# Optimization experiments

Measured on AMD Instinct MI355X. Metric: run time of the kernel, lower is better.

## Reference

```python
import jax, jax.numpy as jnp
import numpy as np
import math

STD = math.exp(0.0025)  # exp(0.5 * 0.005) from log_sigma = 0.005
C = 0.5 * math.log(2 * math.pi)
B, X, H, Z, L, W = 8192, 512, 256, 64, 16, 32

def _predict(h, Wd, bd, Wo, bo):
    return jax.nn.sigmoid(jax.nn.relu(h @ Wd.T + bd) @ Wo.T + bo)

def _gru(xin, h, Wih, Whh, bih, bhh):
    gi = xin @ Wih.T + bih
    gh = h @ Whh.T + bhh
    ir, iz, inn = jnp.split(gi, 3, axis=1)
    hr, hz, hn = jnp.split(gh, 3, axis=1)
    r = jax.nn.sigmoid(ir + hr)
    zt = jax.nn.sigmoid(iz + hz)
    n = jnp.tanh(inn + r * hn)
    return (1.0 - zt) * n + zt * h

def setup_inputs():
    key = jax.random.key(0)
    ks = iter(jax.random.split(key, 40))
    def nrm(shape, s=0.05):
        return jax.random.normal(next(ks), shape, dtype=jnp.float32) * s
    return {
        "x": jax.random.uniform(next(ks), (B, X), dtype=jnp.float32),
        "workers": jax.random.uniform(next(ks), (W, B, L), dtype=jnp.float32),
        "Wf1": nrm((H, X)), "bf1": jnp.zeros((H,)),
        "Wf2": nrm((1, H)), "bf2": jnp.zeros((1,)),
        "eWih": nrm((L, 3 * H, X + 1)), "eWhh": nrm((L, 3 * H, H)),
        "ebih": jnp.zeros((L, 3 * H)), "ebhh": jnp.zeros((L, 3 * H)),
        "eWd": nrm((L, H, H)), "ebd": jnp.zeros((L, H)),
        "eWo": nrm((L, 1, H)), "ebo": jnp.zeros((L, 1)),
        "Wmu": nrm((Z, H)), "bmu": jnp.zeros((Z,)),
        "Wlv": nrm((Z, H)), "blv": jnp.zeros((Z,)),
        "dWih": nrm((L, 3 * H, Z + 1)), "dWhh": nrm((L, 3 * H, H)),
        "dbih": jnp.zeros((L, 3 * H)), "dbhh": jnp.zeros((L, 3 * H)),
        "dWd": nrm((L, H, H)), "dbd": jnp.zeros((L, H)),
        "dWo": nrm((L, W, H)), "dbo": jnp.zeros((L, W)),
        "Wr": nrm((X, H)), "br": jnp.zeros((X,)),
        "enc_eps": jax.random.normal(next(ks), (L, B, H), dtype=jnp.float32),
        "samp_eps": jax.random.normal(next(ks), (B, Z), dtype=jnp.float32),
        "dec_eps": jax.random.uniform(next(ks), (L, B, H), dtype=jnp.float32),
    }

def _forward(x, workers, Wf1, bf1, Wf2, bf2, eWih, eWhh, ebih, ebhh, eWd, ebd, eWo, ebo,
             Wmu, bmu, Wlv, blv, dWih, dWhh, dbih, dbhh, dWd, dbd, dWo, dbo, Wr, br,
             enc_eps, samp_eps, dec_eps):
    nB = x.shape[0]
    h_dim = eWhh.shape[2]
    # Encoder: t[:,0] = firstcell(x)
    t0 = _predict(x, Wf1, bf1, Wf2, bf2)[:, 0]
    z0 = jnp.zeros((nB, h_dim), dtype=x.dtype)

    def enc_step(carry, xs):
        z, ti = carry
        Wih, Whh, bih, bhh, Wd, bd, Wo, bo, eps = xs
        tmp = (ti >= 0.5).astype(x.dtype)
        mu = _gru(jnp.concatenate([x, tmp[:, None]], axis=1), z, Wih, Whh, bih, bhh)
        znew = mu + STD * eps
        tn = _predict(znew, Wd, bd, Wo, bo)[:, 0]
        return (znew, tn), ti

    (z_fin, _), tcols = jax.lax.scan(
        enc_step, (z0, t0), (eWih, eWhh, ebih, ebhh, eWd, ebd, eWo, ebo, enc_eps))
    t = tcols.T  # [B, L]
    mu_z = z_fin @ Wmu.T + bmu
    log_var = jax.nn.softplus(z_fin @ Wlv.T + blv)
    latent = mu_z + jnp.exp(0.5 * log_var) * samp_eps
    tmp_t = (t > 0.5).astype(x.dtype)

    def dec_step(zt, xs):
        Wih, Whh, bih, bhh, Wd, bd, Wo, bo, tcol, eps = xs
        mu = _gru(jnp.concatenate([latent, tcol[:, None]], axis=1), zt, Wih, Whh, bih, bhh)
        znew = mu + STD * eps  # decoder uses uniform eps (torch.rand)
        return znew, _predict(znew, Wd, bd, Wo, bo)

    zT, preds = jax.lax.scan(
        dec_step, jnp.zeros((nB, h_dim), dtype=x.dtype),
        (dWih, dWhh, dbih, dbhh, dWd, dbd, dWo, dbo, tmp_t.T, dec_eps))
    worker_preds = jnp.transpose(preds, (2, 1, 0))  # [L,B,W] -> [W,B,L]
    recon = jax.nn.sigmoid(zT @ Wr.T + br)
    log_p_x = jnp.sum(x * jnp.log(recon), axis=1)
    logp = jnp.clip(jnp.log(worker_preds), -100.0)
    log1mp = jnp.clip(jnp.log1p(-worker_preds), -100.0)
    bce = -(workers * logp + (1.0 - workers) * log1mp)
    log_p_y = -jnp.sum(jnp.sum(bce, axis=0), axis=1)
    workers_bar = jnp.mean(workers, axis=0)
    log_kl = jnp.sum(t * (jnp.log(t + 1e-6) - jnp.log(workers_bar + 1e-6)), axis=1)
    log_p_z = jnp.sum(-C - latent ** 2 / 2, axis=-1)
    log_q = jnp.sum(-C - log_var / 2 - (latent - mu_z) ** 2 / (2 * jnp.exp(log_var)), axis=-1)
    loss = jnp.mean(log_q - log_p_z - log_p_y - log_p_x + log_kl)
    return t, loss

def reference(x, workers, Wf1, bf1, Wf2, bf2, eWih, eWhh, ebih, ebhh, eWd, ebd, eWo, ebo,
              Wmu, bmu, Wlv, blv, dWih, dWhh, dbih, dbhh, dWd, dbd, dWo, dbo, Wr, br,
              enc_eps, samp_eps, dec_eps):
    return _forward(x, workers, Wf1, bf1, Wf2, bf2, eWih, eWhh, ebih, ebhh, eWd, ebd,
                    eWo, ebo, Wmu, bmu, Wlv, blv, dWih, dWhh, dbih, dbhh, dWd, dbd,
                    dWo, dbo, Wr, br, enc_eps, samp_eps, dec_eps)
```

## Files before the change

### kernel.cpp

```cpp
#include <hip/hip_runtime.h>
#include <hip/hip_bf16.h>
#include <math.h>

#define B_ 8192
#define X_ 512
#define H_ 256
#define Z_ 64
#define L_ 16
#define W_ 32
#define G3_ 768

#define STDF 1.0025031276057952f
#define CC 0.9189385332046727f

typedef _Float16 f16x8 __attribute__((ext_vector_type(8)));
typedef float f32x4 __attribute__((ext_vector_type(4)));

__device__ __forceinline__ float sigm(float x) { return 1.0f / (1.0f + expf(-x)); }
__device__ __forceinline__ float logsig(float u) {
    return (u > 0.0f) ? -log1pf(expf(-u)) : (u - log1pf(expf(u)));
}

#define GLOAD16(gsrc, ldst) \
    __builtin_amdgcn_global_load_lds((const __attribute__((address_space(1))) unsigned int*)(gsrc), \
                                     (__attribute__((address_space(3))) unsigned int*)(ldst), 16, 0, 0)

#define WAITV(N) asm volatile("s_waitcnt vmcnt(" #N ")" ::: "memory")
#define SBAR()  do { __builtin_amdgcn_sched_barrier(0); __builtin_amdgcn_s_barrier(); } while (0)

template<int BN>
__global__ __launch_bounds__(256) void mfma_gemm(
    const _Float16* __restrict__ A,
    const _Float16* __restrict__ Wt,
    const float* __restrict__ bias,
    float* __restrict__ C, int ldc,
    int K, int act)
{
    constexpr int BM = 128;
    constexpr int WN = BN / 2;
    constexpr int NFR = WN / 16;
    __shared__ char smem[2][(BM + BN) * 128];

    const int tid  = threadIdx.x;
    const int wave = tid >> 6;
    const int lane = tid & 63;
    const int wr   = wave >> 1;
    const int wc   = wave & 1;
    const int bm   = blockIdx.y * BM;
    const int bn   = blockIdx.x * BN;
    const int l15  = lane & 15;
    const int l4   = lane >> 4;

    f32x4 acc[4][NFR];
    #pragma unroll
    for (int a = 0; a < 4; ++a)
        #pragma unroll
        for (int b = 0; b < NFR; ++b) {
            f32x4 zz = {0.f, 0.f, 0.f, 0.f};
            acc[a][b] = zz;
        }

    auto stage = [&](int s, int pb) {
        char* As = smem[pb];
        char* Ws = smem[pb] + BM * 128;
        int k0 = s * 64;
        #pragma unroll
        for (int it = 0; it < 4; ++it) {
            int q   = it * 4 + wave;
            int o   = q * 1024 + lane * 16;
            int row = o >> 7;
            int c   = ((o >> 4) & 7) ^ (row & 7);
            GLOAD16(A + (long)(bm + row) * K + k0 + c * 8, As + q * 1024);
        }
        #pragma unroll
        for (int it = 0; it < BN / 32; ++it) {
            int q   = it * 4 + wave;
            int o   = q * 1024 + lane * 16;
            int row = o >> 7;
            int c   = ((o >> 4) & 7) ^ (row & 7);
            GLOAD16(Wt + (long)(bn + row) * K + k0 + c * 8, Ws + q * 1024);
        }
    };

    const int NT = K >> 6;
    stage(0, 0);
    for (int s = 0; s < NT; ++s) {
        int pb = s & 1;
        if (s + 1 < NT) {
            stage(s + 1, pb ^ 1);
            if constexpr (BN == 128) WAITV(8); else WAITV(6);
        } else WAITV(0);
        SBAR();
        char* As = smem[pb];
        char* Ws = smem[pb] + BM * 128;
        #pragma unroll
        for (int ks = 0; ks < 2; ++ks) {
            f16x8 af[4], bf[NFR];
            #pragma unroll
            for (int mi = 0; mi < 4; ++mi) {
                int row = wr * 64 + mi * 16 + l15;
                int c   = (ks * 4 + l4) ^ (row & 7);
                af[mi] = *(const f16x8*)(As + row * 128 + c * 16);
            }
            #pragma unroll
            for (int ni = 0; ni < NFR; ++ni) {
                int row = wc * WN + ni * 16 + l15;
                int c   = (ks * 4 + l4) ^ (row & 7);
                bf[ni] = *(const f16x8*)(Ws + row * 128 + c * 16);
            }
            #pragma unroll
            for (int mi = 0; mi < 4; ++mi)
                #pragma unroll
                for (int ni = 0; ni < NFR; ++ni)
                    acc[mi][ni] = __builtin_amdgcn_mfma_f32_16x16x32_f16(
                        af[mi], bf[ni], acc[mi][ni], 0, 0, 0);
        }
        SBAR();
    }

    #pragma unroll
    for (int mi = 0; mi < 4; ++mi)
        #pragma unroll
        for (int r = 0; r < 4; ++r) {
            int grow = bm + wr * 64 + mi * 16 + l4 * 4 + r;
            #pragma unroll
            for (int ni = 0; ni < NFR; ++ni) {
                int gcol = bn + wc * WN + ni * 16 + l15;
                float v = acc[mi][ni][r] + bias[gcol];
                if (act) v = fmaxf(v, 0.0f);
                C[(long)grow * ldc + gcol] = v;
            }
        }
}

template<int MODE, int KX, int FIRST>
__global__ __launch_bounds__(256) void gru_fused(
    const _Float16* __restrict__ A2,
    const _Float16* __restrict__ Wih,
    const float* __restrict__ bih,
    const _Float16* __restrict__ Whh,
    const float* __restrict__ bhh,
    const float* __restrict__ ec,
    const float* __restrict__ tcol,
    const float* __restrict__ eps,
    const _Float16* __restrict__ zh_in,
    float* __restrict__ z,
    _Float16* __restrict__ zh_out)
{
    constexpr int N1 = KX / 64;
    constexpr int NT = N1 + (FIRST ? 0 : 4);
    __shared__ char smem[2][(64 + 192) * 128];

    const int tid  = threadIdx.x;
    const int wave = tid >> 6;
    const int lane = tid & 63;
    const int wr   = wave >> 1;
    const int wc   = wave & 1;
    const int id   = blockIdx.x;
    const int xcd  = id & 7;
    const int wk   = id >> 3;
    const int bm   = (xcd * 16 + (wk >> 2)) * 64;
    const int h0   = (wk & 3) * 64;
    const int l15  = lane & 15;
    const int l4   = lane >> 4;

    f32x4 acc[2][6];
    f32x4 accN[2][2];
    #pragma unroll
    for (int a = 0; a < 2; ++a) {
        #pragma unroll
        for (int b = 0; b < 6; ++b) { f32x4 zz = {0.f,0.f,0.f,0.f}; acc[a][b] = zz; }
        #pragma unroll
        for (int b = 0; b < 2; ++b) { f32x4 zz = {0.f,0.f,0.f,0.f}; accN[a][b] = zz; }
    }

    auto stage = [&](int s, int pb) {
        char* As = smem[pb];
        char* Ws = smem[pb] + 64 * 128;
        const _Float16* srcA;
        const _Float16* srcW;
        int KA, k0;
        if (s < N1) { srcA = A2;    srcW = Wih; KA = KX;  k0 = s * 64; }
        else        { srcA = zh_in; srcW = Whh; KA = 256; k0 = (s - N1) * 64; }
        #pragma unroll
        for (int it = 0; it < 2; ++it) {
            int q   = it * 4 + wave;
            int o   = q * 1024 + lane * 16;
            int row = o >> 7;
            int c   = ((o >> 4) & 7) ^ (row & 7);
            GLOAD16(srcA + (long)(bm + row) * KA + k0 + c * 8, As + q * 1024);
        }
        #pragma unroll
        for (int it = 0; it < 6; ++it) {
            int q   = it * 4 + wave;
            int o   = q * 1024 + lane * 16;
            int rr  = o >> 7;
            int c   = ((o >> 4) & 7) ^ (rr & 7);
            int srow = (rr >> 6) * 256 + h0 + (rr & 63);
            GLOAD16(srcW + (long)srow * KA + k0 + c * 8, Ws + q * 1024);
        }
    };

    stage(0, 0);
    for (int s = 0; s < NT; ++s) {
        int pb = s & 1;
        if (s + 1 < NT) { stage(s + 1, pb ^ 1); WAITV(8); }
        else WAITV(0);
        SBAR();
        char* As = smem[pb];
        char* Ws = smem[pb] + 64 * 128;
        bool p1 = (s < N1);
        #pragma unroll
        for (int ks = 0; ks < 2; ++ks) {
            f16x8 af[2], bf[6];
            #pragma unroll
            for (int mi = 0; mi < 2; ++mi) {
                int row = wr * 32 + mi * 16 + l15;
                int c   = (ks * 4 + l4) ^ (row & 7);
                af[mi] = *(const f16x8*)(As + row * 128 + c * 16);
            }
            #pragma unroll
            for (int ni = 0; ni < 6; ++ni) {
                int rr = (ni >> 1) * 64 + wc * 32 + (ni & 1) * 16 + l15;
                int c  = (ks * 4 + l4) ^ (rr & 7);
                bf[ni] = *(const f16x8*)(Ws + rr * 128 + c * 16);
            }
            if (p1) {
                #pragma unroll
                for (int mi = 0; mi < 2; ++mi) {
                    #pragma unroll
                    for (int ni = 0; ni < 4; ++ni)
                        acc[mi][ni] = __builtin_amdgcn_mfma_f32_16x16x32_f16(
                            af[mi], bf[ni], acc[mi][ni], 0, 0, 0);
                    #pragma unroll
                    for (int ni = 4; ni < 6; ++ni)
                        accN[mi][ni - 4] = __builtin_amdgcn_mfma_f32_16x16x32_f16(
                            af[mi], bf[ni], accN[mi][ni - 4], 0, 0, 0);
                }
            } else {
                #pragma unroll
                for (int mi = 0; mi < 2; ++mi)
                    #pragma unroll
                    for (int ni = 0; ni < 6; ++ni)
                        acc[mi][ni] = __builtin_amdgcn_mfma_f32_16x16x32_f16(
                            af[mi], bf[ni], acc[mi][ni], 0, 0, 0);
            }
        }
        SBAR();
    }

    #pragma unroll
    for (int mi = 0; mi < 2; ++mi)
        #pragma unroll
        for (int r = 0; r < 4; ++r) {
            int grow = bm + wr * 32 + mi * 16 + l4 * 4 + r;
            float tv = tcol[(long)grow * L_];
            float ext = (MODE == 1) ? (tv >= 0.5f ? 1.0f : 0.0f)
                                    : (tv >  0.5f ? 1.0f : 0.0f);
            #pragma unroll
            for (int hb = 0; hb < 2; ++hb) {
                int h = h0 + wc * 32 + hb * 16 + l15;
                float rpre = acc[mi][hb][r]     + bih[h]       + bhh[h]       + ext * ec[h];
                float zpre = acc[mi][2 + hb][r] + bih[256 + h] + bhh[256 + h] + ext * ec[256 + h];
                float hn   = acc[mi][4 + hb][r] + bhh[512 + h];
                float in_  = accN[mi][hb][r]    + bih[512 + h] + ext * ec[512 + h];
                float rg = sigm(rpre);
                float zt = sigm(zpre);
                float n  = tanhf(in_ + rg * hn);
                long zi = (long)grow * 256 + h;
                float zold = FIRST ? 0.0f : z[zi];
                float v = (1.0f - zt) * n + zt * zold + STDF * eps[zi];
                z[zi] = v;
                zh_out[zi] = (_Float16)v;
            }
        }
}

template<int K>
__global__ __launch_bounds__(256) void predict_head(
    const _Float16* __restrict__ A,
    const _Float16* __restrict__ Wd,
    const float* __restrict__ bd,
    const float* __restrict__ wo,
    const float* __restrict__ bo,
    float* __restrict__ out, int ostride)
{
    constexpr int NT = K / 64;
    __shared__ char smem[2][(32 + 256) * 128];
    __shared__ float part[32][4];

    const int tid  = threadIdx.x;
    const int wave = tid >> 6;
    const int lane = tid & 63;
    const int bm   = blockIdx.x * 32;
    const int l15  = lane & 15;
    const int l4   = lane >> 4;

    f32x4 acc[2][4];
    #pragma unroll
    for (int a = 0; a < 2; ++a)
        #pragma unroll
        for (int b = 0; b < 4; ++b) { f32x4 zz = {0.f,0.f,0.f,0.f}; acc[a][b] = zz; }

    auto stage = [&](int s, int pb) {
        char* As = smem[pb];
        char* Ws = smem[pb] + 32 * 128;
        int k0 = s * 64;
        {
            int o   = wave * 1024 + lane * 16;
            int row = o >> 7;
            int c   = ((o >> 4) & 7) ^ (row & 7);
            GLOAD16(A + (long)(bm + row) * K + k0 + c * 8, As + wave * 1024);
        }
        #pragma unroll
        for (int it = 0; it < 8; ++it) {
            int q   = it * 4 + wave;
            int o   = q * 1024 + lane * 16;
            int row = o >> 7;
            int c   = ((o >> 4) & 7) ^ (row & 7);
            GLOAD16(Wd + (long)row * K + k0 + c * 8, Ws + q * 1024);
        }
    };

    stage(0, 0);
    for (int s = 0; s < NT; ++s) {
        int pb = s & 1;
        if (s + 1 < NT) { stage(s + 1, pb ^ 1); WAITV(9); }
        else WAITV(0);
        SBAR();
        char* As = smem[pb];
        char* Ws = smem[pb] + 32 * 128;
        #pragma unroll
        for (int ks = 0; ks < 2; ++ks) {
            f16x8 af[2], bf[4];
            #pragma unroll
            for (int mi = 0; mi < 2; ++mi) {
                int row = mi * 16 + l15;
                int c   = (ks * 4 + l4) ^ (row & 7);
                af[mi] = *(const f16x8*)(As + row * 128 + c * 16);
            }
            #pragma unroll
            for (int ni = 0; ni < 4; ++ni) {
                int row = wave * 64 + ni * 16 + l15;
                int c   = (ks * 4 + l4) ^ (row & 7);
                bf[ni] = *(const f16x8*)(Ws + row * 128 + c * 16);
            }
            #pragma unroll
            for (int mi = 0; mi < 2; ++mi)
                #pragma unroll
                for (int ni = 0; ni < 4; ++ni)
                    acc[mi][ni] = __builtin_amdgcn_mfma_f32_16x16x32_f16(
                        af[mi], bf[ni], acc[mi][ni], 0, 0, 0);
        }
        SBAR();
    }

    float bdv[4], wov[4];
    #pragma unroll
    for (int ni = 0; ni < 4; ++ni) {
        int col = wave * 64 + ni * 16 + l15;
        bdv[ni] = bd[col];
        wov[ni] = wo[col];
    }
    #pragma unroll
    for (int mi = 0; mi < 2; ++mi)
        #pragma unroll
        for (int r = 0; r < 4; ++r) {
            float s = 0.0f;
            #pragma unroll
            for (int ni = 0; ni < 4; ++ni) {
                float v = fmaxf(acc[mi][ni][r] + bdv[ni], 0.0f);
                s = fmaf(v, wov[ni], s);
            }
            #pragma unroll
            for (int off = 1; off < 16; off <<= 1) s += __shfl_xor(s, off, 16);
            if (l15 == 0) part[mi * 16 + l4 * 4 + r][wave] = s;
        }
    __syncthreads();
    if (tid < 32) {
        float u = part[tid][0] + part[tid][1] + part[tid][2] + part[tid][3] + bo[0];
        out[(long)(bm + tid) * ostride] = sigm(u);
    }
}

__global__ __launch_bounds__(256) void dec_head_bce(
    const _Float16* __restrict__ A,
    const _Float16* __restrict__ Wd,
    const float* __restrict__ bd,
    const _Float16* __restrict__ Wo,
    const float* __restrict__ bo,
    const float* __restrict__ wt,
    float* __restrict__ bacc)
{
    constexpr int NT = 4;
    __shared__ char smem[2][(32 + 256) * 128];
    __shared__ _Float16 ds[32 * 264];
    __shared__ float part[32][2];

    const int tid  = threadIdx.x;
    const int wave = tid >> 6;
    const int lane = tid & 63;
    const int bm   = blockIdx.x * 32;
    const int l15  = lane & 15;
    const int l4   = lane >> 4;

    f32x4 acc[2][4];
    #pragma unroll
    for (int a = 0; a < 2; ++a)
        #pragma unroll
        for (int b = 0; b < 4; ++b) { f32x4 zz = {0.f,0.f,0.f,0.f}; acc[a][b] = zz; }

    auto stage = [&](int s, int pb) {
        char* As = smem[pb];
        char* Ws = smem[pb] + 32 * 128;
        int k0 = s * 64;
        {
            int o   = wave * 1024 + lane * 16;
            int row = o >> 7;
            int c   = ((o >> 4) & 7) ^ (row & 7);
            GLOAD16(A + (long)(bm + row) * 256 + k0 + c * 8, As + wave * 1024);
        }
        #pragma unroll
        for (int it = 0; it < 8; ++it) {
            int q   = it * 4 + wave;
            int o   = q * 1024 + lane * 16;
            int row = o >> 7;
            int c   = ((o >> 4) & 7) ^ (row & 7);
            GLOAD16(Wd + (long)row * 256 + k0 + c * 8, Ws + q * 1024);
        }
    };

    stage(0, 0);
    for (int s = 0; s < NT; ++s) {
        int pb = s & 1;
        if (s + 1 < NT) { stage(s + 1, pb ^ 1); WAITV(9); }
        else WAITV(0);
        SBAR();
        char* As = smem[pb];
        char* Ws = smem[pb] + 32 * 128;
        #pragma unroll
        for (int ks = 0; ks < 2; ++ks) {
            f16x8 af[2], bf[4];
            #pragma unroll
            for (int mi = 0; mi < 2; ++mi) {
                int row = mi * 16 + l15;
                int c   = (ks * 4 + l4) ^ (row & 7);
                af[mi] = *(const f16x8*)(As + row * 128 + c * 16);
            }
            #pragma unroll
            for (int ni = 0; ni < 4; ++ni) {
                int row = wave * 64 + ni * 16 + l15;
                int c   = (ks * 4 + l4) ^ (row & 7);
                bf[ni] = *(const f16x8*)(Ws + row * 128 + c * 16);
            }
            #pragma unroll
            for (int mi = 0; mi < 2; ++mi)
                #pragma unroll
                for (int ni = 0; ni < 4; ++ni)
                    acc[mi][ni] = __builtin_amdgcn_mfma_f32_16x16x32_f16(
                        af[mi], bf[ni], acc[mi][ni], 0, 0, 0);
        }
        SBAR();
    }

    #pragma unroll
    for (int mi = 0; mi < 2; ++mi)
        #pragma unroll
        for (int r = 0; r < 4; ++r) {
            int row = mi * 16 + l4 * 4 + r;
            #pragma unroll
            for (int ni = 0; ni < 4; ++ni) {
                int col = wave * 64 + ni * 16 + l15;
                ds[row * 264 + col] = (_Float16)fmaxf(acc[mi][ni][r] + bd[col], 0.0f);
            }
        }
    __syncthreads();

    const int rh = wave >> 1;
    const int ch = wave & 1;
    f32x4 acc2 = {0.f, 0.f, 0.f, 0.f};
    #pragma unroll
    for (int k = 0; k < 8; ++k) {
        f16x8 bf2 = *(const f16x8*)(Wo + (long)(ch * 16 + l15) * 256 + k * 32 + l4 * 8);
        f16x8 af  = *(const f16x8*)(ds + (rh * 16 + l15) * 264 + k * 32 + l4 * 8);
        acc2 = __builtin_amdgcn_mfma_f32_16x16x32_f16(af, bf2, acc2, 0, 0, 0);
    }

    #pragma unroll
    for (int r = 0; r < 4; ++r) {
        int row = rh * 16 + l4 * 4 + r;
        int w = ch * 16 + l15;
        float u = acc2[r] + bo[w];
        float logp   = fmaxf(logsig(u),  -100.0f);
        float log1mp = fmaxf(logsig(-u), -100.0f);
        float wk = wt[(long)(bm + row) * W_ + w];
        float s = -(wk * logp + (1.0f - wk) * log1mp);
        #pragma unroll
        for (int off = 1; off < 16; off <<= 1) s += __shfl_xor(s, off, 16);
        if (l15 == 0) part[row][ch] = s;
    }
    __syncthreads();
    if (tid < 32) bacc[bm + tid] += part[tid][0] + part[tid][1];
}

__global__ __launch_bounds__(256) void wtrans(
    const float* __restrict__ workers, float* __restrict__ wt,
    float* __restrict__ bacc)
{
    long idx = (long)blockIdx.x * 256 + threadIdx.x;
    int w = idx & 31;
    long b = idx >> 5;
    const float* src = workers + (w * (long)B_ + b) * L_;
    #pragma unroll
    for (int l = 0; l < L_; ++l)
        wt[((long)l * B_ + b) * W_ + w] = src[l];
    if (w == 0) bacc[b] = 0.0f;
}

struct ConvJobs {
    const float* s[10];
    _Float16* d[10];
};
__device__ __constant__ const long CJ_CNT[10] = {
    (long)B_ * X_,
    (long)H_ * X_,
    (long)L_ * G3_ * H_,
    (long)L_ * H_ * H_,
    (long)L_ * G3_ * H_,
    (long)L_ * H_ * H_,
    (long)L_ * W_ * H_,
    (long)X_ * H_,
    (long)Z_ * H_,
    (long)Z_ * H_
};
#define CJ_TOTAL 13008896L

__global__ __launch_bounds__(256) void conv_multi(ConvJobs J)
{
    long i8 = ((long)blockIdx.x * 256 + threadIdx.x) * 8;
    if (i8 >= CJ_TOTAL) return;
    long rem = i8; int j = 0;
    #pragma unroll
    for (int k = 0; k < 9; ++k)
        if (rem >= CJ_CNT[k]) { rem -= CJ_CNT[k]; ++j; } else break;
    const float* s = J.s[j] + rem;
    f16x8 o;
    #pragma unroll
    for (int q = 0; q < 8; ++q) o[q] = (_Float16)s[q];
    *(f16x8*)(J.d[j] + rem) = o;
}

__global__ __launch_bounds__(256) void conv_f16(
    const float* __restrict__ src, _Float16* __restrict__ dst,
    int Ks, int Kd, long total)
{
    long i = ((long)blockIdx.x * 256 + threadIdx.x) * 8;
    if (i >= total) return;
    long r = i / Kd, k = i - r * Kd;
    const float* s = src + r * Ks + k;
    f16x8 o;
    #pragma unroll
    for (int j = 0; j < 8; ++j) o[j] = (_Float16)s[j];
    *(f16x8*)(dst + i) = o;
}

__global__ __launch_bounds__(256) void extract_col(
    const float* __restrict__ src, float* __restrict__ dst, int Ks, int col, int R)
{
    int i = blockIdx.x * 256 + threadIdx.x;
    if (i < R) dst[i] = src[(long)i * Ks + col];
}

__global__ void stack_bias(const float* __restrict__ a, const float* __restrict__ b,
                           float* __restrict__ o)
{
    int i = threadIdx.x;
    o[i] = (i < 64) ? a[i] : b[i - 64];
}

__global__ __launch_bounds__(256) void latent_elem(
    const float* __restrict__ muv,
    const float* __restrict__ seps,
    float* __restrict__ latent, _Float16* __restrict__ lath,
    float* __restrict__ lq, float* __restrict__ lpz)
{
    int wave = threadIdx.x >> 6, lane = threadIdx.x & 63;
    int b = blockIdx.x * 4 + wave;
    float mu = muv[(long)b * 128 + lane];
    float sp = muv[(long)b * 128 + 64 + lane];
    float lv = (sp > 0.0f) ? (sp + log1pf(expf(-sp))) : log1pf(expf(sp));
    float e  = seps[(long)b * Z_ + lane];
    float lat = mu + expf(0.5f * lv) * e;
    latent[(long)b * Z_ + lane] = lat;
    lath[(long)b * Z_ + lane] = (_Float16)lat;
    float lpz_c = -CC - 0.5f * lat * lat;
    float d = lat - mu;
    float lq_c = -CC - 0.5f * lv - d * d / (2.0f * expf(lv));
    #pragma unroll
    for (int off = 32; off; off >>= 1) {
        lpz_c += __shfl_down(lpz_c, off);
        lq_c  += __shfl_down(lq_c, off);
    }
    if (lane == 0) { lpz[b] = lpz_c; lq[b] = lq_c; }
}

__global__ __launch_bounds__(256) void logpx_reduce(
    const float* __restrict__ u, const float* __restrict__ x,
    float* __restrict__ lpx)
{
    int wave = threadIdx.x >> 6, lane = threadIdx.x & 63;
    int b = blockIdx.x * 4 + wave;
    const float* ub = u + (long)b * X_;
    const float* xb = x + (long)b * X_;
    float s = 0.0f;
    #pragma unroll
    for (int i = 0; i < 8; ++i) {
        int k = lane + i * 64;
        s = fmaf(xb[k], logsig(ub[k]), s);
    }
    #pragma unroll
    for (int off = 32; off; off >>= 1) s += __shfl_down(s, off);
    if (lane == 0) lpx[b] = s;
}

__global__ __launch_bounds__(256) void kl_kernel(
    const float* __restrict__ tmat, const float* __restrict__ workers,
    float* __restrict__ lkl)
{
    int b = blockIdx.x * 256 + threadIdx.x;
    float wb[L_];
    #pragma unroll
    for (int l = 0; l < L_; ++l) wb[l] = 0.0f;
    for (int w = 0; w < W_; ++w) {
        const float* p = workers + ((long)w * B_ + b) * L_;
        #pragma unroll
        for (int l = 0; l < L_; ++l) wb[l] += p[l];
    }
    float s = 0.0f;
    #pragma unroll
    for (int l = 0; l < L_; ++l) {
        float wbar = wb[l] * (1.0f / 32.0f);
        float tv = tmat[(long)b * L_ + l];
        s += tv * (logf(tv + 1e-6f) - logf(wbar + 1e-6f));
    }
    lkl[b] = s;
}

__global__ __launch_bounds__(1024) void final_reduce(
    const float* __restrict__ lq, const float* __restrict__ lpz,
    const float* __restrict__ bacc, const float* __restrict__ lpx,
    const float* __restrict__ lkl, float* __restrict__ out)
{
    __shared__ float red[16];
    float s = 0.0f;
    for (int b = threadIdx.x; b < B_; b += 1024)
        s += lq[b] - lpz[b] + bacc[b] - lpx[b] + lkl[b];
    #pragma unroll
    for (int off = 32; off; off >>= 1) s += __shfl_down(s, off);
    int wave = threadIdx.x >> 6, lane = threadIdx.x & 63;
    if (lane == 0) red[wave] = s;
    __syncthreads();
    if (threadIdx.x == 0) {
        float t = 0.0f;
        for (int i = 0; i < 16; ++i) t += red[i];
        out[0] = t / (float)B_;
    }
}

extern "C" void kernel_launch(void* const* d_in, const int* in_sizes, int n_in,
                              void* d_out, int out_size, void* d_ws, size_t ws_size,
                              hipStream_t stream)
{
    const float* x       = (const float*)d_in[0];
    const float* workers = (const float*)d_in[1];
    const float* Wf1     = (const float*)d_in[2];
    const float* bf1     = (const float*)d_in[3];
    const float* Wf2     = (const float*)d_in[4];
    const float* bf2     = (const float*)d_in[5];
    const float* eWih    = (const float*)d_in[6];
    const float* eWhh    = (const float*)d_in[7];
    const float* ebih    = (const float*)d_in[8];
    const float* ebhh    = (const float*)d_in[9];
    const float* eWd     = (const float*)d_in[10];
    const float* ebd     = (const float*)d_in[11];
    const float* eWo     = (const float*)d_in[12];
    const float* ebo     = (const float*)d_in[13];
    const float* Wmu     = (const float*)d_in[14];
    const float* bmu     = (const float*)d_in[15];
    const float* Wlv     = (const float*)d_in[16];
    const float* blv     = (const float*)d_in[17];
    const float* dWih    = (const float*)d_in[18];
    const float* dWhh    = (const float*)d_in[19];
    const float* dbih    = (const float*)d_in[20];
    const float* dbhh    = (const float*)d_in[21];
    const float* dWd     = (const float*)d_in[22];
    const float* dbd     = (const float*)d_in[23];
    const float* dWo     = (const float*)d_in[24];
    const float* dbo     = (const float*)d_in[25];
    const float* Wr      = (const float*)d_in[26];
    const float* br      = (const float*)d_in[27];
    const float* enc_eps = (const float*)d_in[28];
    const float* samp_eps= (const float*)d_in[29];
    const float* dec_eps = (const float*)d_in[30];

    float* t    = (float*)d_out;
    float* loss = t + (long)B_ * L_;

    char* p = (char*)d_ws;
    auto alloc = [&](size_t bytes) {
        char* r = p;
        p += (bytes + 255) & ~(size_t)255;
        return r;
    };
    _Float16* xh    = (_Float16*)alloc((size_t)B_ * X_ * 2);
    _Float16* zha   = (_Float16*)alloc((size_t)B_ * H_ * 2);
    _Float16* zhb   = (_Float16*)alloc((size_t)B_ * H_ * 2);
    _Float16* lath  = (_Float16*)alloc((size_t)B_ * Z_ * 2);
    _Float16* Wf1h  = (_Float16*)alloc((size_t)H_ * X_ * 2);
    _Float16* eWihh = (_Float16*)alloc((size_t)L_ * G3_ * X_ * 2);
    _Float16* eWhhh = (_Float16*)alloc((size_t)L_ * G3_ * H_ * 2);
    _Float16* eWdh  = (_Float16*)alloc((size_t)L_ * H_ * H_ * 2);
    _Float16* dWihh = (_Float16*)alloc((size_t)L_ * G3_ * Z_ * 2);
    _Float16* dWhhh = (_Float16*)alloc((size_t)L_ * G3_ * H_ * 2);
    _Float16* dWdh  = (_Float16*)alloc((size_t)L_ * H_ * H_ * 2);
    _Float16* dWoh  = (_Float16*)alloc((size_t)L_ * W_ * H_ * 2);
    _Float16* Wrh   = (_Float16*)alloc((size_t)X_ * H_ * 2);
    _Float16* Wmlh  = (_Float16*)alloc((size_t)128 * H_ * 2);
    float* bml    = (float*)alloc(128 * 4);
    float* eWihc  = (float*)alloc((size_t)L_ * G3_ * 4);
    float* dWihc  = (float*)alloc((size_t)L_ * G3_ * 4);
    float* z      = (float*)alloc((size_t)B_ * H_ * 4);
    float* dbuf   = (float*)alloc((size_t)B_ * H_ * 4);
    float* latent = (float*)alloc((size_t)B_ * Z_ * 4);
    float* wt     = (float*)alloc((size_t)L_ * B_ * W_ * 4);
    float* logits = (float*)alloc((size_t)B_ * X_ * 4);
    float* lq     = (float*)alloc((size_t)B_ * 4);
    float* lpz    = (float*)alloc((size_t)B_ * 4);
    float* lpx    = (float*)alloc((size_t)B_ * 4);
    float* lkl    = (float*)alloc((size_t)B_ * 4);
    float* bacc   = (float*)alloc((size_t)B_ * 4);

    const dim3 blk(256);
    const int nBH = B_ * H_;
    auto cgrid = [](long total) { return dim3((unsigned)((total / 8 + 255) / 256)); };

    ConvJobs J;
    J.s[0] = x;    J.d[0] = xh;
    J.s[1] = Wf1;  J.d[1] = Wf1h;
    J.s[2] = eWhh; J.d[2] = eWhhh;
    J.s[3] = eWd;  J.d[3] = eWdh;
    J.s[4] = dWhh; J.d[4] = dWhhh;
    J.s[5] = dWd;  J.d[5] = dWdh;
    J.s[6] = dWo;  J.d[6] = dWoh;
    J.s[7] = Wr;   J.d[7] = Wrh;
    J.s[8] = Wmu;  J.d[8] = Wmlh;
    J.s[9] = Wlv;  J.d[9] = Wmlh + (long)Z_ * H_;
    conv_multi<<<(CJ_TOTAL / 8 + 255) / 256, blk, 0, stream>>>(J);
    conv_f16<<<cgrid((long)L_ * G3_ * X_), blk, 0, stream>>>(eWih, eWihh, X_ + 1, X_, (long)L_ * G3_ * X_);
    conv_f16<<<cgrid((long)L_ * G3_ * Z_), blk, 0, stream>>>(dWih, dWihh, Z_ + 1, Z_, (long)L_ * G3_ * Z_);
    stack_bias<<<1, 128, 0, stream>>>(bmu, blv, bml);
    extract_col<<<(L_ * G3_ + 255) / 256, blk, 0, stream>>>(eWih, eWihc, X_ + 1, X_, L_ * G3_);
    extract_col<<<(L_ * G3_ + 255) / 256, blk, 0, stream>>>(dWih, dWihc, Z_ + 1, Z_, L_ * G3_);
    wtrans<<<(W_ * B_) / 256, blk, 0, stream>>>(workers, wt, bacc);

    predict_head<X_><<<B_ / 32, blk, 0, stream>>>(xh, Wf1h, bf1, Wf2, bf2, t, L_);

    _Float16* zcur = zha;
    _Float16* znxt = zhb;
    for (int l = 0; l < L_; ++l) {
        if (l == 0)
            gru_fused<1, X_, 1><<<512, blk, 0, stream>>>(
                xh, eWihh, ebih, eWhhh, ebhh, eWihc, t, enc_eps, zcur, z, znxt);
        else
            gru_fused<1, X_, 0><<<512, blk, 0, stream>>>(
                xh, eWihh + (long)l * G3_ * X_, ebih + (long)l * G3_,
                eWhhh + (long)l * G3_ * H_, ebhh + (long)l * G3_,
                eWihc + (long)l * G3_, t + l, enc_eps + (long)l * nBH,
                zcur, z, znxt);
        _Float16* tmp = zcur; zcur = znxt; znxt = tmp;
        if (l < L_ - 1)
            predict_head<H_><<<B_ / 32, blk, 0, stream>>>(
                zcur, eWdh + (long)l * H_ * H_, ebd + (long)l * H_,
                eWo + (long)l * H_, ebo + l, t + (l + 1), L_);
    }

    mfma_gemm<64><<<dim3(2, B_ / 128), blk, 0, stream>>>(
        zcur, Wmlh, bml, dbuf, 128, H_, 0);
    latent_elem<<<B_ / 4, blk, 0, stream>>>(dbuf, samp_eps, latent, lath, lq, lpz);

    zcur = zha; znxt = zhb;
    for (int l = 0; l < L_; ++l) {
        if (l == 0)
            gru_fused<2, Z_, 1><<<512, blk, 0, stream>>>(
                lath, dWihh, dbih, dWhhh, dbhh, dWihc, t, dec_eps, zcur, z, znxt);
        else
            gru_fused<2, Z_, 0><<<512, blk, 0, stream>>>(
                lath, dWihh + (long)l * G3_ * Z_, dbih + (long)l * G3_,
                dWhhh + (long)l * G3_ * H_, dbhh + (long)l * G3_,
                dWihc + (long)l * G3_, t + l, dec_eps + (long)l * nBH,
                zcur, z, znxt);
        _Float16* tmp = zcur; zcur = znxt; znxt = tmp;
        dec_head_bce<<<B_ / 32, blk, 0, stream>>>(
            zcur, dWdh + (long)l * H_ * H_, dbd + (long)l * H_,
            dWoh + (long)l * W_ * H_, dbo + (long)l * W_,
            wt + (long)l * B_ * W_, bacc);
    }

    mfma_gemm<128><<<dim3(X_ / 128, B_ / 128), blk, 0, stream>>>(
        zcur, Wrh, br, logits, X_, H_, 0);
    logpx_reduce<<<B_ / 4, blk, 0, stream>>>(logits, x, lpx);
    kl_kernel<<<B_ / 256, blk, 0, stream>>>(t, workers, lkl);
    final_reduce<<<1, 1024, 0, stream>>>(lq, lpz, bacc, lpx, lkl, loss);
}
```

Baseline: 1.107 ms.

## Fuse latent and recon-logpx epilogues into GEMMs; load head weights whole into LDS

The latent projection is fused with the reparameterisation and log-density terms, and the reconstruction GEMM is fused with the log-sigmoid reduction using atomics. This drops the intermediate fp32 logits and dbuf buffers and the separate elementwise kernels. The encoder predict head and decoder BCE head now load the full 256x256 weight tile into 128KB of LDS in one shot instead of double-buffered K stages. The large LDS footprint limits occupancy to one block per CU, and the atomic lpx accumulation needs lpx zeroed up front, which is now done in wtrans.

```diff
diff --git a/kernel.cpp b/kernel.cpp
--- a/kernel.cpp
+++ b/kernel.cpp
@@ -27,111 +27,6 @@
 
 #define WAITV(N) asm volatile("s_waitcnt vmcnt(" #N ")" ::: "memory")
 #define SBAR()  do { __builtin_amdgcn_sched_barrier(0); __builtin_amdgcn_s_barrier(); } while (0)
-
-template<int BN>
-__global__ __launch_bounds__(256) void mfma_gemm(
-    const _Float16* __restrict__ A,
-    const _Float16* __restrict__ Wt,
-    const float* __restrict__ bias,
-    float* __restrict__ C, int ldc,
-    int K, int act)
-{
-    constexpr int BM = 128;
-    constexpr int WN = BN / 2;
-    constexpr int NFR = WN / 16;
-    __shared__ char smem[2][(BM + BN) * 128];
-
-    const int tid  = threadIdx.x;
-    const int wave = tid >> 6;
-    const int lane = tid & 63;
-    const int wr   = wave >> 1;
-    const int wc   = wave & 1;
-    const int bm   = blockIdx.y * BM;
-    const int bn   = blockIdx.x * BN;
-    const int l15  = lane & 15;
-    const int l4   = lane >> 4;
-
-    f32x4 acc[4][NFR];
-    #pragma unroll
-    for (int a = 0; a < 4; ++a)
-        #pragma unroll
-        for (int b = 0; b < NFR; ++b) {
-            f32x4 zz = {0.f, 0.f, 0.f, 0.f};
-            acc[a][b] = zz;
-        }
-
-    auto stage = [&](int s, int pb) {
-        char* As = smem[pb];
-        char* Ws = smem[pb] + BM * 128;
-        int k0 = s * 64;
-        #pragma unroll
-        for (int it = 0; it < 4; ++it) {
-            int q   = it * 4 + wave;
-            int o   = q * 1024 + lane * 16;
-            int row = o >> 7;
-            int c   = ((o >> 4) & 7) ^ (row & 7);
-            GLOAD16(A + (long)(bm + row) * K + k0 + c * 8, As + q * 1024);
-        }
-        #pragma unroll
-        for (int it = 0; it < BN / 32; ++it) {
-            int q   = it * 4 + wave;
-            int o   = q * 1024 + lane * 16;
-            int row = o >> 7;
-            int c   = ((o >> 4) & 7) ^ (row & 7);
-            GLOAD16(Wt + (long)(bn + row) * K + k0 + c * 8, Ws + q * 1024);
-        }
-    };
-
-    const int NT = K >> 6;
-    stage(0, 0);
-    for (int s = 0; s < NT; ++s) {
-        int pb = s & 1;
-        if (s + 1 < NT) {
-            stage(s + 1, pb ^ 1);
-            if constexpr (BN == 128) WAITV(8); else WAITV(6);
-        } else WAITV(0);
-        SBAR();
-        char* As = smem[pb];
-        char* Ws = smem[pb] + BM * 128;
-        #pragma unroll
-        for (int ks = 0; ks < 2; ++ks) {
-            f16x8 af[4], bf[NFR];
-            #pragma unroll
-            for (int mi = 0; mi < 4; ++mi) {
-                int row = wr * 64 + mi * 16 + l15;
-                int c   = (ks * 4 + l4) ^ (row & 7);
-                af[mi] = *(const f16x8*)(As + row * 128 + c * 16);
-            }
-            #pragma unroll
-            for (int ni = 0; ni < NFR; ++ni) {
-                int row = wc * WN + ni * 16 + l15;
-                int c   = (ks * 4 + l4) ^ (row & 7);
-                bf[ni] = *(const f16x8*)(Ws + row * 128 + c * 16);
-            }
-            #pragma unroll
-            for (int mi = 0; mi < 4; ++mi)
-                #pragma unroll
-                for (int ni = 0; ni < NFR; ++ni)
-                    acc[mi][ni] = __builtin_amdgcn_mfma_f32_16x16x32_f16(
-                        af[mi], bf[ni], acc[mi][ni], 0, 0, 0);
-        }
-        SBAR();
-    }
-
-    #pragma unroll
-    for (int mi = 0; mi < 4; ++mi)
-        #pragma unroll
-        for (int r = 0; r < 4; ++r) {
-            int grow = bm + wr * 64 + mi * 16 + l4 * 4 + r;
-            #pragma unroll
-            for (int ni = 0; ni < NFR; ++ni) {
-                int gcol = bn + wc * WN + ni * 16 + l15;
-                float v = acc[mi][ni][r] + bias[gcol];
-                if (act) v = fmaxf(v, 0.0f);
-                C[(long)grow * ldc + gcol] = v;
-            }
-        }
-}
 
 template<int MODE, int KX, int FIRST>
 __global__ __launch_bounds__(256) void gru_fused(
@@ -276,8 +171,7 @@
         }
 }
 
-template<int K>
-__global__ __launch_bounds__(256) void predict_head(
+__global__ __launch_bounds__(256) void predict_head512(
     const _Float16* __restrict__ A,
     const _Float16* __restrict__ Wd,
     const float* __restrict__ bd,
@@ -285,6 +179,7 @@
     const float* __restrict__ bo,
     float* __restrict__ out, int ostride)
 {
+    constexpr int K = 512;
     constexpr int NT = K / 64;
     __shared__ char smem[2][(32 + 256) * 128];
     __shared__ float part[32][4];
@@ -383,7 +278,106 @@
     }
 }
 
-__global__ __launch_bounds__(256) void dec_head_bce(
+__global__ __launch_bounds__(256) void predict_fast(
+    const _Float16* __restrict__ A,
+    const _Float16* __restrict__ Wd,
+    const float* __restrict__ bd,
+    const float* __restrict__ wo,
+    const float* __restrict__ bo,
+    float* __restrict__ out, int ostride)
+{
+    __shared__ char Wl[131072];
+    __shared__ char Al[16384];
+    __shared__ float part[32][4];
+
+    const int tid  = threadIdx.x;
+    const int wave = tid >> 6;
+    const int lane = tid & 63;
+    const int bm   = blockIdx.x * 32;
+    const int l15  = lane & 15;
+    const int l4   = lane >> 4;
+
+    #pragma unroll
+    for (int q = 0; q < 32; ++q) {
+        int f   = q * 4096 + tid * 16;
+        int kc  = f >> 15;
+        int o   = f & 32767;
+        int row = o >> 7;
+        int c   = ((o >> 4) & 7) ^ (row & 7);
+        GLOAD16(Wd + (long)row * 256 + kc * 64 + c * 8, Wl + f);
+    }
+    #pragma unroll
+    for (int q = 0; q < 4; ++q) {
+        int f   = q * 4096 + tid * 16;
+        int kc  = f >> 12;
+        int o   = f & 4095;
+        int row = o >> 7;
+        int c   = ((o >> 4) & 7) ^ (row & 7);
+        GLOAD16(A + (long)(bm + row) * 256 + kc * 64 + c * 8, Al + f);
+    }
+    WAITV(0);
+    __syncthreads();
+
+    f32x4 acc[2][4];
+    #pragma unroll
+    for (int a = 0; a < 2; ++a)
+        #pragma unroll
+        for (int b = 0; b < 4; ++b) { f32x4 zz = {0.f,0.f,0.f,0.f}; acc[a][b] = zz; }
+
+    #pragma unroll
+    for (int kc = 0; kc < 4; ++kc)
+        #pragma unroll
+        for (int ks = 0; ks < 2; ++ks) {
+            f16x8 af[2], bf[4];
+            #pragma unroll
+            for (int mi = 0; mi < 2; ++mi) {
+                int row = mi * 16 + l15;
+                int c   = (ks * 4 + l4) ^ (row & 7);
+                af[mi] = *(const f16x8*)(Al + kc * 4096 + row * 128 + c * 16);
+            }
+            #pragma unroll
+            for (int ni = 0; ni < 4; ++ni) {
+                int row = wave * 64 + ni * 16 + l15;
+                int c   = (ks * 4 + l4) ^ (row & 7);
+                bf[ni] = *(const f16x8*)(Wl + kc * 32768 + row * 128 + c * 16);
+            }
+            #pragma unroll
+            for (int mi = 0; mi < 2; ++mi)
+                #pragma unroll
+                for (int ni = 0; ni < 4; ++ni)
+                    acc[mi][ni] = __builtin_amdgcn_mfma_f32_16x16x32_f16(
+                        af[mi], bf[ni], acc[mi][ni], 0, 0, 0);
+        }
+
+    float bdv[4], wov[4];
+    #pragma unroll
+    for (int ni = 0; ni < 4; ++ni) {
+        int col = wave * 64 + ni * 16 + l15;
+        bdv[ni] = bd[col];
+        wov[ni] = wo[col];
+    }
+    #pragma unroll
+    for (int mi = 0; mi < 2; ++mi)
+        #pragma unroll
+        for (int r = 0; r < 4; ++r) {
+            float s = 0.0f;
+            #pragma unroll
+            for (int ni = 0; ni < 4; ++ni) {
+                float v = fmaxf(acc[mi][ni][r] + bdv[ni], 0.0f);
+                s = fmaf(v, wov[ni], s);
+            }
+            #pragma unroll
+            for (int off = 1; off < 16; off <<= 1) s += __shfl_xor(s, off, 16);
+            if (l15 == 0) part[mi * 16 + l4 * 4 + r][wave] = s;
+        }
+    __syncthreads();
+    if (tid < 32) {
+        float u = part[tid][0] + part[tid][1] + part[tid][2] + part[tid][3] + bo[0];
+        out[(long)(bm + tid) * ostride] = sigm(u);
+    }
+}
+
+__global__ __launch_bounds__(256) void dec_head_bce_fast(
     const _Float16* __restrict__ A,
     const _Float16* __restrict__ Wd,
     const float* __restrict__ bd,
@@ -392,8 +386,7 @@
     const float* __restrict__ wt,
     float* __restrict__ bacc)
 {
-    constexpr int NT = 4;
-    __shared__ char smem[2][(32 + 256) * 128];
+    __shared__ char Wl[131072];
     __shared__ _Float16 ds[32 * 264];
     __shared__ float part[32][2];
 
@@ -404,63 +397,71 @@
     const int l15  = lane & 15;
     const int l4   = lane >> 4;
 
+    #pragma unroll
+    for (int q = 0; q < 32; ++q) {
+        int f   = q * 4096 + tid * 16;
+        int kc  = f >> 15;
+        int o   = f & 32767;
+        int row = o >> 7;
+        int c   = ((o >> 4) & 7) ^ (row & 7);
+        GLOAD16(Wd + (long)row * 256 + kc * 64 + c * 8, Wl + f);
+    }
+    f16x8 afr[8];
+    #pragma unroll
+    for (int kc = 0; kc < 4; ++kc)
+        #pragma unroll
+        for (int mi = 0; mi < 2; ++mi) {
+            int row = mi * 16 + l15;
+            afr[kc * 2 + mi] = *(const f16x8*)(A + (long)(bm + row) * 256 + kc * 64 + l4 * 8);
+        }
+
     f32x4 acc[2][4];
     #pragma unroll
     for (int a = 0; a < 2; ++a)
         #pragma unroll
         for (int b = 0; b < 4; ++b) { f32x4 zz = {0.f,0.f,0.f,0.f}; acc[a][b] = zz; }
 
-    auto stage = [&](int s, int pb) {
-        char* As = smem[pb];
-        char* Ws = smem[pb] + 32 * 128;
-        int k0 = s * 64;
-        {
-            int o   = wave * 1024 + lane * 16;
-            int row = o >> 7;
-            int c   = ((o >> 4) & 7) ^ (row & 7);
-            GLOAD16(A + (long)(bm + row) * 256 + k0 + c * 8, As + wave * 1024);
-        }
-        #pragma unroll
-        for (int it = 0; it < 8; ++it) {
-            int q   = it * 4 + wave;
-            int o   = q * 1024 + lane * 16;
-            int row = o >> 7;
-            int c   = ((o >> 4) & 7) ^ (row & 7);
-            GLOAD16(Wd + (long)row * 256 + k0 + c * 8, Ws + q * 1024);
-        }
-    };
-
-    stage(0, 0);
-    for (int s = 0; s < NT; ++s) {
-        int pb = s & 1;
-        if (s + 1 < NT) { stage(s + 1, pb ^ 1); WAITV(9); }
-        else WAITV(0);
-        SBAR();
-        char* As = smem[pb];
-        char* Ws = smem[pb] + 32 * 128;
-        #pragma unroll
-        for (int ks = 0; ks < 2; ++ks) {
-            f16x8 af[2], bf[4];
-            #pragma unroll
-            for (int mi = 0; mi < 2; ++mi) {
-                int row = mi * 16 + l15;
-                int c   = (ks * 4 + l4) ^ (row & 7);
-                af[mi] = *(const f16x8*)(As + row * 128 + c * 16);
-            }
-            #pragma unroll
-            for (int ni = 0; ni < 4; ++ni) {
-                int row = wave * 64 + ni * 16 + l15;
-                int c   = (ks * 4 + l4) ^ (row & 7);
-                bf[ni] = *(const f16x8*)(Ws + row * 128 + c * 16);
-            }
-            #pragma unroll
-            for (int mi = 0; mi < 2; ++mi)
-                #pragma unroll
-                for (int ni = 0; ni < 4; ++ni)
-                    acc[mi][ni] = __builtin_amdgcn_mfma_f32_16x16x32_f16(
-                        af[mi], bf[ni], acc[mi][ni], 0, 0, 0);
-        }
-        SBAR();
+    WAITV(0);
+    __syncthreads();
+
+    #pragma unroll
+    for (int kc = 0; kc < 4; ++kc) {
+        f16x8 bf[4];
+        #pragma unroll
+        for (int ni = 0; ni < 4; ++ni) {
+            int row = wave * 64 + ni * 16 + l15;
+            int c   = (0 * 4 + l4) ^ (row & 7);
+            bf[ni] = *(const f16x8*)(Wl + kc * 32768 + row * 128 + c * 16);
+        }
+        #pragma unroll
+        for (int mi = 0; mi < 2; ++mi)
+            #pragma unroll
+            for (int ni = 0; ni < 4; ++ni)
+                acc[mi][ni] = __builtin_amdgcn_mfma_f32_16x16x32_f16(
+                    afr[kc * 2 + mi], bf[ni], acc[mi][ni], 0, 0, 0);
+    }
+    #pragma unroll
+    for (int kc = 0; kc < 4; ++kc)
+        #pragma unroll
+        for (int mi = 0; mi < 2; ++mi) {
+            int row = mi * 16 + l15;
+            afr[kc * 2 + mi] = *(const f16x8*)(A + (long)(bm + row) * 256 + kc * 64 + 32 + l4 * 8);
+        }
+    #pragma unroll
+    for (int kc = 0; kc < 4; ++kc) {
+        f16x8 bf[4];
+        #pragma unroll
+        for (int ni = 0; ni < 4; ++ni) {
+            int row = wave * 64 + ni * 16 + l15;
+            int c   = (1 * 4 + l4) ^ (row & 7);
+            bf[ni] = *(const f16x8*)(Wl + kc * 32768 + row * 128 + c * 16);
+        }
+        #pragma unroll
+        for (int mi = 0; mi < 2; ++mi)
+            #pragma unroll
+            for (int ni = 0; ni < 4; ++ni)
+                acc[mi][ni] = __builtin_amdgcn_mfma_f32_16x16x32_f16(
+                    afr[kc * 2 + mi], bf[ni], acc[mi][ni], 0, 0, 0);
     }
 
     #pragma unroll
@@ -503,9 +504,221 @@
     if (tid < 32) bacc[bm + tid] += part[tid][0] + part[tid][1];
 }
 
+__global__ __launch_bounds__(256) void latent_fused(
+    const _Float16* __restrict__ A,
+    const _Float16* __restrict__ Wml,
+    const float* __restrict__ bml,
+    const float* __restrict__ seps,
+    _Float16* __restrict__ lath,
+    float* __restrict__ lq, float* __restrict__ lpz)
+{
+    __shared__ char Wl[65536];
+    __shared__ char Al[16384];
+    __shared__ float muv[32][129];
+
+    const int tid  = threadIdx.x;
+    const int wave = tid >> 6;
+    const int lane = tid & 63;
+    const int bm   = blockIdx.x * 32;
+    const int l15  = lane & 15;
+    const int l4   = lane >> 4;
+
+    #pragma unroll
+    for (int q = 0; q < 16; ++q) {
+        int f   = q * 4096 + tid * 16;
+        int kc  = f >> 14;
+        int o   = f & 16383;
+        int row = o >> 7;
+        int c   = ((o >> 4) & 7) ^ (row & 7);
+        GLOAD16(Wml + (long)row * 256 + kc * 64 + c * 8, Wl + f);
+    }
+    #pragma unroll
+    for (int q = 0; q < 4; ++q) {
+        int f   = q * 4096 + tid * 16;
+        int kc  = f >> 12;
+        int o   = f & 4095;
+        int row = o >> 7;
+        int c   = ((o >> 4) & 7) ^ (row & 7);
+        GLOAD16(A + (long)(bm + row) * 256 + kc * 64 + c * 8, Al + f);
+    }
+    WAITV(0);
+    __syncthreads();
+
+    f32x4 acc[2][2];
+    #pragma unroll
+    for (int a = 0; a < 2; ++a)
+        #pragma unroll
+        for (int b = 0; b < 2; ++b) { f32x4 zz = {0.f,0.f,0.f,0.f}; acc[a][b] = zz; }
+
+    #pragma unroll
+    for (int kc = 0; kc < 4; ++kc)
+        #pragma unroll
+        for (int ks = 0; ks < 2; ++ks) {
+            f16x8 af[2], bf[2];
+            #pragma unroll
+            for (int mi = 0; mi < 2; ++mi) {
+                int row = mi * 16 + l15;
+                int c   = (ks * 4 + l4) ^ (row & 7);
+                af[mi] = *(const f16x8*)(Al + kc * 4096 + row * 128 + c * 16);
+            }
+            #pragma unroll
+            for (int ni = 0; ni < 2; ++ni) {
+                int row = wave * 32 + ni * 16 + l15;
+                int c   = (ks * 4 + l4) ^ (row & 7);
+                bf[ni] = *(const f16x8*)(Wl + kc * 16384 + row * 128 + c * 16);
+            }
+            #pragma unroll
+            for (int mi = 0; mi < 2; ++mi)
+                #pragma unroll
+                for (int ni = 0; ni < 2; ++ni)
+                    acc[mi][ni] = __builtin_amdgcn_mfma_f32_16x16x32_f16(
+                        af[mi], bf[ni], acc[mi][ni], 0, 0, 0);
+        }
+
+    #pragma unroll
+    for (int mi = 0; mi < 2; ++mi)
+        #pragma unroll
+        for (int r = 0; r < 4; ++r) {
+            int row = mi * 16 + l4 * 4 + r;
+            #pragma unroll
+            for (int ni = 0; ni < 2; ++ni) {
+                int col = wave * 32 + ni * 16 + l15;
+                muv[row][col] = acc[mi][ni][r] + bml[col];
+            }
+        }
+    __syncthreads();
+
+    int rsub = lane >> 3;
+    int row  = wave * 8 + rsub;
+    int zlo  = lane & 7;
+    float lpz_c = 0.0f, lq_c = 0.0f;
+    #pragma unroll
+    for (int j = 0; j < 8; ++j) {
+        int zc = zlo * 8 + j;
+        float mu = muv[row][zc];
+        float sp = muv[row][64 + zc];
+        float lv = (sp > 0.0f) ? (sp + log1pf(expf(-sp))) : log1pf(expf(sp));
+        float e  = seps[(long)(bm + row) * Z_ + zc];
+        float lat = mu + expf(0.5f * lv) * e;
+        lath[(long)(bm + row) * Z_ + zc] = (_Float16)lat;
+        lpz_c += -CC - 0.5f * lat * lat;
+        float d = lat - mu;
+        lq_c += -CC - 0.5f * lv - d * d / (2.0f * expf(lv));
+    }
+    #pragma unroll
+    for (int off = 1; off < 8; off <<= 1) {
+        lpz_c += __shfl_xor(lpz_c, off, 8);
+        lq_c  += __shfl_xor(lq_c, off, 8);
+    }
+    if (zlo == 0) { lpz[bm + row] = lpz_c; lq[bm + row] = lq_c; }
+}
+
+__global__ __launch_bounds__(256) void recon_logpx_gemm(
+    const _Float16* __restrict__ A,
+    const _Float16* __restrict__ Wt,
+    const float* __restrict__ bias,
+    const float* __restrict__ x,
+    float* __restrict__ lpx)
+{
+    constexpr int K = 256;
+    constexpr int NT = 4;
+    __shared__ char smem[2][(128 + 128) * 128];
+    __shared__ float part[128][2];
+
+    const int tid  = threadIdx.x;
+    const int wave = tid >> 6;
+    const int lane = tid & 63;
+    const int wr   = wave >> 1;
+    const int wc   = wave & 1;
+    const int bm   = blockIdx.y * 128;
+    const int bn   = blockIdx.x * 128;
+    const int l15  = lane & 15;
+    const int l4   = lane >> 4;
+
+    f32x4 acc[4][4];
+    #pragma unroll
+    for (int a = 0; a < 4; ++a)
+        #pragma unroll
+        for (int b = 0; b < 4; ++b) { f32x4 zz = {0.f,0.f,0.f,0.f}; acc[a][b] = zz; }
+
+    auto stage = [&](int s, int pb) {
+        char* As = smem[pb];
+        char* Ws = smem[pb] + 128 * 128;
+        int k0 = s * 64;
+        #pragma unroll
+        for (int it = 0; it < 4; ++it) {
+            int q   = it * 4 + wave;
+            int o   = q * 1024 + lane * 16;
+            int row = o >> 7;
+            int c   = ((o >> 4) & 7) ^ (row & 7);
+            GLOAD16(A + (long)(bm + row) * K + k0 + c * 8, As + q * 1024);
+        }
+        #pragma unroll
+        for (int it = 0; it < 4; ++it) {
+            int q   = it * 4 + wave;
+            int o   = q * 1024 + lane * 16;
+            int row = o >> 7;
+            int c   = ((o >> 4) & 7) ^ (row & 7);
+            GLOAD16(Wt + (long)(bn + row) * K + k0 + c * 8, Ws + q * 1024);
+        }
+    };
+
+    stage(0, 0);
+    for (int s = 0; s < NT; ++s) {
+        int pb = s & 1;
+        if (s + 1 < NT) { stage(s + 1, pb ^ 1); WAITV(8); }
+        else WAITV(0);
+        SBAR();
+        char* As = smem[pb];
+        char* Ws = smem[pb] + 128 * 128;
+        #pragma unroll
+        for (int ks = 0; ks < 2; ++ks) {
+            f16x8 af[4], bf[4];
+            #pragma unroll
+            for (int mi = 0; mi < 4; ++mi) {
+                int row = wr * 64 + mi * 16 + l15;
+                int c   = (ks * 4 + l4) ^ (row & 7);
+                af[mi] = *(const f16x8*)(As + row * 128 + c * 16);
+            }
+            #pragma unroll
+            for (int ni = 0; ni < 4; ++ni) {
+                int row = wc * 64 + ni * 16 + l15;
+                int c   = (ks * 4 + l4) ^ (row & 7);
+                bf[ni] = *(const f16x8*)(Ws + row * 128 + c * 16);
+            }
+            #pragma unroll
+            for (int mi = 0; mi < 4; ++mi)
+                #pragma unroll
+                for (int ni = 0; ni < 4; ++ni)
+                    acc[mi][ni] = __builtin_amdgcn_mfma_f32_16x16x32_f16(
+                        af[mi], bf[ni], acc[mi][ni], 0, 0, 0);
+        }
+        SBAR();
+    }
+
+    #pragma unroll
+    for (int mi = 0; mi < 4; ++mi)
+        #pragma unroll
+        for (int r = 0; r < 4; ++r) {
+            int grow = bm + wr * 64 + mi * 16 + l4 * 4 + r;
+            float s = 0.0f;
+            #pragma unroll
+            for (int ni = 0; ni < 4; ++ni) {
+                int gcol = bn + wc * 64 + ni * 16 + l15;
+                float u = acc[mi][ni][r] + bias[gcol];
+                s = fmaf(x[(long)grow * X_ + gcol], logsig(u), s);
+            }
+            #pragma unroll
+            for (int off = 1; off < 16; off <<= 1) s += __shfl_xor(s, off, 16);
+            if (l15 == 0) part[wr * 64 + mi * 16 + l4 * 4 + r][wc] = s;
+        }
+    __syncthreads();
+    if (tid < 128) atomicAdd(&lpx[bm + tid], part[tid][0] + part[tid][1]);
+}
+
 __global__ __launch_bounds__(256) void wtrans(
     const float* __restrict__ workers, float* __restrict__ wt,
-    float* __restrict__ bacc)
+    float* __restrict__ bacc, float* __restrict__ lpx)
 {
     long idx = (long)blockIdx.x * 256 + threadIdx.x;
     int w = idx & 31;
@@ -514,7 +727,7 @@
     #pragma unroll
     for (int l = 0; l < L_; ++l)
         wt[((long)l * B_ + b) * W_ + w] = src[l];
-    if (w == 0) bacc[b] = 0.0f;
+    if (w == 0) { bacc[b] = 0.0f; lpx[b] = 0.0f; }
 }
 
 struct ConvJobs {
@@ -522,16 +735,9 @@
     _Float16* d[10];
 };
 __device__ __constant__ const long CJ_CNT[10] = {
-    (long)B_ * X_,
-    (long)H_ * X_,
-    (long)L_ * G3_ * H_,
-    (long)L_ * H_ * H_,
-    (long)L_ * G3_ * H_,
-    (long)L_ * H_ * H_,
-    (long)L_ * W_ * H_,
-    (long)X_ * H_,
-    (long)Z_ * H_,
-    (long)Z_ * H_
+    (long)B_ * X_, (long)H_ * X_, (long)L_ * G3_ * H_, (long)L_ * H_ * H_,
+    (long)L_ * G3_ * H_, (long)L_ * H_ * H_, (long)L_ * W_ * H_,
+    (long)X_ * H_, (long)Z_ * H_, (long)Z_ * H_
 };
 #define CJ_TOTAL 13008896L
 
@@ -576,51 +782,6 @@
 {
     int i = threadIdx.x;
     o[i] = (i < 64) ? a[i] : b[i - 64];
-}
-
-__global__ __launch_bounds__(256) void latent_elem(
-    const float* __restrict__ muv,
-    const float* __restrict__ seps,
-    float* __restrict__ latent, _Float16* __restrict__ lath,
-    float* __restrict__ lq, float* __restrict__ lpz)
-{
-    int wave = threadIdx.x >> 6, lane = threadIdx.x & 63;
-    int b = blockIdx.x * 4 + wave;
-    float mu = muv[(long)b * 128 + lane];
-    float sp = muv[(long)b * 128 + 64 + lane];
-    float lv = (sp > 0.0f) ? (sp + log1pf(expf(-sp))) : log1pf(expf(sp));
-    float e  = seps[(long)b * Z_ + lane];
-    float lat = mu + expf(0.5f * lv) * e;
-    latent[(long)b * Z_ + lane] = lat;
-    lath[(long)b * Z_ + lane] = (_Float16)lat;
-    float lpz_c = -CC - 0.5f * lat * lat;
-    float d = lat - mu;
-    float lq_c = -CC - 0.5f * lv - d * d / (2.0f * expf(lv));
-    #pragma unroll
-    for (int off = 32; off; off >>= 1) {
-        lpz_c += __shfl_down(lpz_c, off);
-        lq_c  += __shfl_down(lq_c, off);
-    }
-    if (lane == 0) { lpz[b] = lpz_c; lq[b] = lq_c; }
-}
-
-__global__ __launch_bounds__(256) void logpx_reduce(
-    const float* __restrict__ u, const float* __restrict__ x,
-    float* __restrict__ lpx)
-{
-    int wave = threadIdx.x >> 6, lane = threadIdx.x & 63;
-    int b = blockIdx.x * 4 + wave;
-    const float* ub = u + (long)b * X_;
-    const float* xb = x + (long)b * X_;
-    float s = 0.0f;
-    #pragma unroll
-    for (int i = 0; i < 8; ++i) {
-        int k = lane + i * 64;
-        s = fmaf(xb[k], logsig(ub[k]), s);
-    }
-    #pragma unroll
-    for (int off = 32; off; off >>= 1) s += __shfl_down(s, off);
-    if (lane == 0) lpx[b] = s;
 }
 
 __global__ __launch_bounds__(256) void kl_kernel(
@@ -730,10 +891,7 @@
     float* eWihc  = (float*)alloc((size_t)L_ * G3_ * 4);
     float* dWihc  = (float*)alloc((size_t)L_ * G3_ * 4);
     float* z      = (float*)alloc((size_t)B_ * H_ * 4);
-    float* dbuf   = (float*)alloc((size_t)B_ * H_ * 4);
-    float* latent = (float*)alloc((size_t)B_ * Z_ * 4);
     float* wt     = (float*)alloc((size_t)L_ * B_ * W_ * 4);
-    float* logits = (float*)alloc((size_t)B_ * X_ * 4);
     float* lq     = (float*)alloc((size_t)B_ * 4);
     float* lpz    = (float*)alloc((size_t)B_ * 4);
     float* lpx    = (float*)alloc((size_t)B_ * 4);
@@ -761,9 +919,9 @@
     stack_bias<<<1, 128, 0, stream>>>(bmu, blv, bml);
     extract_col<<<(L_ * G3_ + 255) / 256, blk, 0, stream>>>(eWih, eWihc, X_ + 1, X_, L_ * G3_);
     extract_col<<<(L_ * G3_ + 255) / 256, blk, 0, stream>>>(dWih, dWihc, Z_ + 1, Z_, L_ * G3_);
-    wtrans<<<(W_ * B_) / 256, blk, 0, stream>>>(workers, wt, bacc);
-
-    predict_head<X_><<<B_ / 32, blk, 0, stream>>>(xh, Wf1h, bf1, Wf2, bf2, t, L_);
+    wtrans<<<(W_ * B_) / 256, blk, 0, stream>>>(workers, wt, bacc, lpx);
+
+    predict_head512<<<B_ / 32, blk, 0, stream>>>(xh, Wf1h, bf1, Wf2, bf2, t, L_);
 
     _Float16* zcur = zha;
     _Float16* znxt = zhb;
@@ -779,14 +937,12 @@
                 zcur, z, znxt);
         _Float16* tmp = zcur; zcur = znxt; znxt = tmp;
         if (l < L_ - 1)
-            predict_head<H_><<<B_ / 32, blk, 0, stream>>>(
+            predict_fast<<<B_ / 32, blk, 0, stream>>>(
                 zcur, eWdh + (long)l * H_ * H_, ebd + (long)l * H_,
                 eWo + (long)l * H_, ebo + l, t + (l + 1), L_);
     }
 
-    mfma_gemm<64><<<dim3(2, B_ / 128), blk, 0, stream>>>(
-        zcur, Wmlh, bml, dbuf, 128, H_, 0);
-    latent_elem<<<B_ / 4, blk, 0, stream>>>(dbuf, samp_eps, latent, lath, lq, lpz);
+    latent_fused<<<B_ / 32, blk, 0, stream>>>(zcur, Wmlh, bml, samp_eps, lath, lq, lpz);
 
     zcur = zha; znxt = zhb;
     for (int l = 0; l < L_; ++l) {
@@ -800,15 +956,14 @@
                 dWihc + (long)l * G3_, t + l, dec_eps + (long)l * nBH,
                 zcur, z, znxt);
         _Float16* tmp = zcur; zcur = znxt; znxt = tmp;
-        dec_head_bce<<<B_ / 32, blk, 0, stream>>>(
+        dec_head_bce_fast<<<B_ / 32, blk, 0, stream>>>(
             zcur, dWdh + (long)l * H_ * H_, dbd + (long)l * H_,
             dWoh + (long)l * W_ * H_, dbo + (long)l * W_,
             wt + (long)l * B_ * W_, bacc);
     }
 
-    mfma_gemm<128><<<dim3(X_ / 128, B_ / 128), blk, 0, stream>>>(
-        zcur, Wrh, br, logits, X_, H_, 0);
-    logpx_reduce<<<B_ / 4, blk, 0, stream>>>(logits, x, lpx);
+    recon_logpx_gemm<<<dim3(X_ / 128, B_ / 128), blk, 0, stream>>>(
+        zcur, Wrh, br, x, lpx);
     kl_kernel<<<B_ / 256, blk, 0, stream>>>(t, workers, lkl);
     final_reduce<<<1, 1024, 0, stream>>>(lq, lpz, bacc, lpx, lkl, loss);
 }
```

Measured after the change: 1.111 ms. Within noise of the previous version (+0.4%).
